# Optimization experiments

Measured on AMD Instinct MI355X. Metric: run time of the kernel, lower is better.

Reference implementation:

```python
import jax, jax.numpy as jnp
import numpy as np
from jax import lax

DEPTH = 3
L = 2 ** DEPTH          # n_leaves
N_NODES = 2 ** DEPTH - 1
B, C, H, W = 256, 3, 32, 32
OC = 64
K = 3
OUT_WIDTH = 10
INPUT_WIDTH = C * H * W
FC_IN = OC * H * W // 4


def setup_inputs() -> dict:
    key = jax.random.key(0)
    ks = jax.random.split(key, 9)
    f1 = 1.0 / np.sqrt(INPUT_WIDTH)
    u = lambda k, shape, f: jax.random.uniform(k, shape, jnp.float32, -f, f)
    fcf = 1.0 / np.sqrt(FC_IN)
    return {
        "x": jax.random.normal(ks[0], (B, C, H, W), jnp.float32),
        "node_weights": u(ks[1], (N_NODES, INPUT_WIDTH), f1),
        "node_biases": u(ks[2], (N_NODES, 1), f1),
        "cw1s": u(ks[3], (L, OC, C, K, K), f1),
        "cb1s": u(ks[4], (L, OC), f1),
        "cw2s": u(ks[5], (L, OC, OC, K, K), f1),
        "cb2s": u(ks[6], (L, OC), f1),
        "fc_w": u(ks[7], (OUT_WIDTH, FC_IN), fcf),
        "fc_b": u(ks[8], (OUT_WIDTH,), fcf),
    }


def _soft_mixture(xf, node_weights, node_biases):
    # xf: [B, C*H*W] -> per-sample mixture over leaves [B, L]
    b = xf.shape[0]
    mixture = jnp.ones((b, L), xf.dtype)
    for d in range(DEPTH):  # fixed small structural loop over tree depth
        p0, p1 = 2 ** d - 1, 2 ** (d + 1) - 1
        n = 2 ** d
        logits = xf @ node_weights[p0:p1].T + node_biases[p0:p1].T  # [B, n]
        be = jax.nn.sigmoid(logits)
        mod = jnp.stack([1.0 - be, be], axis=-1).reshape(b, 2 * n, 1)
        mixture = (mixture.reshape(b, 2 * n, L // (2 * n)) * mod).reshape(b, L)
    return mixture


def reference(x, node_weights, node_biases, cw1s, cb1s, cw2s, cb2s, fc_w, fc_b):
    b = x.shape[0]
    xf = x.reshape(b, -1)
    mixture = _soft_mixture(xf, node_weights, node_biases)  # [B, L]

    pad = K // 2  # 'same' padding for odd kernel, stride 1
    # conv1 for all leaves at once: stack leaf kernels along output channels
    w1 = cw1s.reshape(L * OC, C, K, K)
    y = lax.conv_general_dilated(x, w1, (1, 1), [(pad, pad), (pad, pad)])
    y = y + cb1s.reshape(1, L * OC, 1, 1)            # [B, L*OC, H, W]
    y = lax.reduce_window(y, -jnp.inf, lax.max, (1, 1, 2, 2), (1, 1, 2, 2), "VALID")
    y = jax.nn.relu(y)                                # [B, L*OC, H/2, W/2]
    # conv2 as grouped conv (one group per leaf)
    w2 = cw2s.reshape(L * OC, OC, K, K)
    y = lax.conv_general_dilated(y, w2, (1, 1), [(pad, pad), (pad, pad)],
                                 feature_group_count=L)
    y = jax.nn.relu(y + cb2s.reshape(1, L * OC, 1, 1))
    y = y.reshape(b, L, OC, H // 2, W // 2)
    out = jnp.einsum("bl,blchw->bchw", mixture, y)    # mixture-weighted sum over leaves
    flat = out.reshape(b, -1)
    return flat @ fc_w.T + fc_b                       # [B, OUT_WIDTH]
```

## Files before the change

### kernel.cpp

```cpp
#include <hip/hip_runtime.h>
#include <cstdint>
#include <cstddef>

#define B_ 256
#define IW_ 3072
#define L_ 8
#define NN_ 7
#define FCIN_ 16384
#define OUTW_ 10
#define ICST 40
#define YPLANE (324 * ICST)

typedef short short8 __attribute__((ext_vector_type(8)));
typedef float f32x4 __attribute__((ext_vector_type(4)));

__device__ __forceinline__ ushort f2bf(float x) {
    uint u = __float_as_uint(x);
    return (ushort)((u + 0x7fffu + ((u >> 16) & 1u)) >> 16);
}
__device__ __forceinline__ float bf2f(ushort b) { return __uint_as_float(((uint)b) << 16); }

__global__ __launch_bounds__(256) void k_prep(const float* __restrict__ w1, ushort* __restrict__ w1fr,
                                              const float* __restrict__ w2, ushort* __restrict__ w2r,
                                              const float* __restrict__ x, const float* __restrict__ nw,
                                              const float* __restrict__ nb, float* __restrict__ mix) {
    int blk = blockIdx.x;
    if (blk < 64) {
        int i = blk * 256 + threadIdx.x;
        int j    = i & 7;
        int lane = (i >> 3) & 63;
        int mt   = (i >> 9) & 3;
        int l    = i >> 11;
        int fr = lane & 15, fq = lane >> 4;
        int oc = mt * 16 + fr;
        int k = fq * 8 + j;
        float w = (k < 27) ? w1[(size_t)(l * 64 + oc) * 27 + k] : 0.f;
        w1fr[i] = f2bf(w);
        return;
    }
    if (blk < 1216) {
        int i = (blk - 64) * 256 + threadIdx.x;
        int j     = i & 7;
        int lane  = (i >> 3) & 63;
        int mt    = (i >> 9) & 3;
        int tap   = (i >> 11) % 9;
        int icc   = (i / 18432) & 1;
        int l     = i / 36864;
        int fr = lane & 15, fq = lane >> 4;
        int oc = mt * 16 + fr;
        int ic = icc * 32 + fq * 8 + j;
        float w = w2[(((size_t)l * 64 + oc) * 64 + ic) * 9 + tap];
        w2r[i] = f2bf(w);
        return;
    }
    __shared__ float red[4 * NN_];
    __shared__ float bes[NN_];
    int b = blk - 1216, tid = threadIdx.x;
    const float* xb = x + (size_t)b * IW_;
    float p[NN_];
#pragma unroll
    for (int n = 0; n < NN_; ++n) p[n] = 0.f;
    for (int i = tid; i < IW_; i += 256) {
        float xv = xb[i];
#pragma unroll
        for (int n = 0; n < NN_; ++n) p[n] = fmaf(xv, nw[n * IW_ + i], p[n]);
    }
#pragma unroll
    for (int n = 0; n < NN_; ++n) {
        float v = p[n];
        for (int off = 32; off > 0; off >>= 1) v += __shfl_xor(v, off);
        if ((tid & 63) == 0) red[(tid >> 6) * NN_ + n] = v;
    }
    __syncthreads();
    if (tid < NN_) {
        float s = red[tid] + red[NN_ + tid] + red[2 * NN_ + tid] + red[3 * NN_ + tid] + nb[tid];
        bes[tid] = 1.f / (1.f + expf(-s));
    }
    __syncthreads();
    if (tid < L_) {
        int leaf = tid;
        float b0 = bes[0];
        float t0 = ((leaf >> 2) & 1) ? b0 : 1.f - b0;
        float b1v = bes[1 + ((leaf >> 2) & 1)];
        float t1 = ((leaf >> 1) & 1) ? b1v : 1.f - b1v;
        float b2v = bes[3 + ((leaf >> 1) & 3)];
        float t2 = (leaf & 1) ? b2v : 1.f - b2v;
        mix[b * L_ + leaf] = t0 * t1 * t2;
    }
}

__global__ __launch_bounds__(1024, 1) void k_fused(const float* __restrict__ x,
                                                   const ushort* __restrict__ w1fr,
                                                   const float* __restrict__ cb1,
                                                   const ushort* __restrict__ w2r,
                                                   const float* __restrict__ cb2, const float* __restrict__ mixw,
                                                   float* __restrict__ out1, int boff) {
    __shared__ __align__(16) ushort smem[2 * YPLANE];
    float* xpad = (float*)smem;

    int tid = threadIdx.x;
    int bl = blockIdx.x;
    int b = boff + bl;
    int lane = tid & 63, wid = tid >> 6;
    int fr = lane & 15, fq = lane >> 4;
    int mt = wid >> 2, ng = wid & 3;

    for (int i = tid; i < 3 * 34 * 34; i += 1024) xpad[i] = 0.f;
    __syncthreads();
    for (int i = tid; i < 3072; i += 1024) {
        int ch = i >> 10, rr = (i >> 5) & 31, cc = i & 31;
        xpad[(ch * 34 + rr + 1) * 34 + cc + 1] = x[(size_t)b * IW_ + i];
    }
    __syncthreads();

    short8 Bh[4];
#pragma unroll
    for (int i = 0; i < 4; ++i) {
        int subrow = i >> 1;
        int parity = i & 1;
        int prow = wid * 2 + subrow;
        int pcol = 2 * fr + parity;
#pragma unroll
        for (int j = 0; j < 8; ++j) {
            int k = fq * 8 + j;
            float xv = 0.f;
            if (k < 27) {
                int ic = k / 9;
                int tap = k - ic * 9;
                int dr = tap / 3, dc = tap - dr * 3;
                xv = xpad[(ic * 34 + prow + dr) * 34 + (pcol + dc)];
            }
            Bh[i][j] = (short)f2bf(xv);
        }
    }
    __syncthreads();
    {
        uint4 z; z.x = z.y = z.z = z.w = 0u;
        for (int i = tid; i < (2 * YPLANE) / 8; i += 1024) ((uint4*)smem)[i] = z;
    }
    __syncthreads();

    f32x4 acc[4], oacc[4];
#pragma unroll
    for (int rl = 0; rl < 4; ++rl) { acc[rl] = (f32x4)0.f; oacc[rl] = (f32x4)0.f; }

    auto CONV1 = [&](int s) {
        int l = s >> 1, icc = s & 1;
        ushort* yt = smem + (size_t)(s & 1) * YPLANE;
#pragma unroll
        for (int mt2 = 0; mt2 < 2; ++mt2) {
            int mtg = icc * 2 + mt2;
            short8 ah = *(const short8*)(w1fr + ((size_t)(l * 4 + mtg) * 64 + lane) * 8);
            f32x4 a1[4];
#pragma unroll
            for (int i = 0; i < 4; ++i) {
                f32x4 t = (f32x4)0.f;
                t = __builtin_amdgcn_mfma_f32_16x16x32_bf16(ah, Bh[i], t, 0, 0, 0);
                a1[i] = t;
            }
            float4 bias4 = *(const float4*)(cb1 + l * 64 + mtg * 16 + fq * 4);
            float bb[4] = {bias4.x, bias4.y, bias4.z, bias4.w};
            ushort hb[4];
#pragma unroll
            for (int j2 = 0; j2 < 4; ++j2) {
                float m0 = fmaxf(fmaxf(a1[0][j2], a1[1][j2]), fmaxf(a1[2][j2], a1[3][j2]));
                float v = fmaxf(m0 + bb[j2], 0.f);
                hb[j2] = f2bf(v);
            }
            int off = ((wid + 1) * 18 + (fr + 1)) * ICST + mt2 * 16 + fq * 4;
            uint2 H;
            H.x = (uint)hb[0] | ((uint)hb[1] << 16);
            H.y = (uint)hb[2] | ((uint)hb[3] << 16);
            *(uint2*)&yt[off] = H;
        }
    };

    auto CONV2 = [&](int s) {
        int l = s >> 1, icc = s & 1;
        const ushort* yt = smem + (size_t)(s & 1) * YPLANE;
        const ushort* wbase = w2r + (size_t)(l * 2 + icc) * 18432;
#pragma unroll
        for (int dc = 0; dc < 3; ++dc) {
            short8 Ah[3];
#pragma unroll
            for (int dr = 0; dr < 3; ++dr) {
                int tap = dr * 3 + dc;
                Ah[dr] = *(const short8*)(wbase + ((size_t)(tap * 4 + mt) * 64 + lane) * 8);
            }
#pragma unroll
            for (int rr = 0; rr < 6; ++rr) {
                int off = ((4 * ng + rr) * 18 + (fr + dc)) * ICST + fq * 8;
                short8 bh = *(const short8*)(yt + off);
#pragma unroll
                for (int dr = 0; dr < 3; ++dr) {
                    int rl = rr - dr;
                    if (rl >= 0 && rl < 4) {
                        acc[rl] = __builtin_amdgcn_mfma_f32_16x16x32_bf16(Ah[dr], bh, acc[rl], 0, 0, 0);
                    }
                }
            }
        }
        if (icc) {
            float mx = mixw[(size_t)b * 8 + l];
#pragma unroll
            for (int j = 0; j < 4; ++j) {
                float bias = cb2[l * 64 + mt * 16 + fq * 4 + j];
#pragma unroll
                for (int rl = 0; rl < 4; ++rl) {
                    float v = fmaxf(acc[rl][j] + bias, 0.f);
                    oacc[rl][j] = fmaf(mx, v, oacc[rl][j]);
                    acc[rl][j] = 0.f;
                }
            }
        }
    };

    CONV1(0);
    __syncthreads();
    for (int s = 0; s < 16; ++s) {
        if (s < 15) CONV1(s + 1);
        CONV2(s);
        __syncthreads();
    }

#pragma unroll
    for (int rl = 0; rl < 4; ++rl)
#pragma unroll
        for (int j = 0; j < 4; ++j) {
            int oc = mt * 16 + fq * 4 + j;
            int pos = (4 * ng + rl) * 16 + fr;
            out1[((size_t)bl * 64 + oc) * 256 + pos] = oacc[rl][j];
        }
}

__global__ __launch_bounds__(256) void k_fc(const float* __restrict__ out1, const float* __restrict__ fcw,
                                            const float* __restrict__ fcb, float* __restrict__ out, int boff) {
    __shared__ float red[4][OUTW_];
    int tid = threadIdx.x;
    int bl = blockIdx.x;
    const float4* flat = (const float4*)(out1 + (size_t)bl * FCIN_);
    float pj[OUTW_];
#pragma unroll
    for (int j = 0; j < OUTW_; ++j) pj[j] = 0.f;
    for (int i = tid; i < FCIN_ / 4; i += 256) {
        float4 v = flat[i];
#pragma unroll
        for (int j = 0; j < OUTW_; ++j) {
            float4 w = ((const float4*)(fcw + (size_t)j * FCIN_))[i];
            pj[j] += v.x * w.x + v.y * w.y + v.z * w.z + v.w * w.w;
        }
    }
#pragma unroll
    for (int j = 0; j < OUTW_; ++j) {
        float v = pj[j];
        for (int off = 32; off > 0; off >>= 1) v += __shfl_xor(v, off);
        if ((tid & 63) == 0) red[tid >> 6][j] = v;
    }
    __syncthreads();
    if (tid < OUTW_) {
        float s = red[0][tid] + red[1][tid] + red[2][tid] + red[3][tid] + fcb[tid];
        out[(size_t)(boff + bl) * OUTW_ + tid] = s;
    }
}

extern "C" void kernel_launch(void* const* d_in, const int* in_sizes, int n_in,
                              void* d_out, int out_size, void* d_ws, size_t ws_size,
                              hipStream_t stream) {
    const float* x   = (const float*)d_in[0];
    const float* nw  = (const float*)d_in[1];
    const float* nb  = (const float*)d_in[2];
    const float* w1  = (const float*)d_in[3];
    const float* cb1 = (const float*)d_in[4];
    const float* w2  = (const float*)d_in[5];
    const float* cb2 = (const float*)d_in[6];
    const float* fcw = (const float*)d_in[7];
    const float* fcb = (const float*)d_in[8];
    float* out = (float*)d_out;

    float*  ws   = (float*)d_ws;
    float*  mix  = ws;
    ushort* w1fr = (ushort*)(mix + 2048);
    ushort* w2r  = w1fr + 16384;
    float*  out1 = (float*)(w2r + 294912);

    long avail = (long)ws_size - 630784L;
    int Bc = (int)(avail / 65536L);
    if (Bc > B_) Bc = B_;
    if (Bc < 1) Bc = 1;

    k_prep<<<1472, 256, 0, stream>>>(w1, w1fr, w2, w2r, x, nw, nb, mix);

    for (int boff = 0; boff < B_; boff += Bc) {
        int bc = (B_ - boff < Bc) ? (B_ - boff) : Bc;
        k_fused<<<bc, 1024, 0, stream>>>(x, w1fr, cb1, w2r, cb2, mix, out1, boff);
        k_fc<<<bc, 256, 0, stream>>>(out1, fcw, fcb, out, boff);
    }
}
```

Before: 80.30 us.

## Fuse FC into conv kernel and process full leaf per pipeline stage

Computes all 64 conv1 channels per leaf into a wider LDS tile, so the software pipeline runs 8 leaf stages instead of 16 half-channel stages and needs half as many barriers. The FC layer is moved into the fused kernel: the mixture-weighted output is staged in LDS and dotted against fc weights there, which removes the global out1 round trip, the separate k_fc launch and the batch-chunk loop. In exchange it uses more LDS per block, and each block now does its own FC weight streaming.

```diff
diff --git a/kernel.cpp b/kernel.cpp
--- a/kernel.cpp
+++ b/kernel.cpp
@@ -8,7 +8,7 @@
 #define NN_ 7
 #define FCIN_ 16384
 #define OUTW_ 10
-#define ICST 40
+#define ICST 72
 #define YPLANE (324 * ICST)
 
 typedef short short8 __attribute__((ext_vector_type(8)));
@@ -94,13 +94,13 @@
                                                    const float* __restrict__ cb1,
                                                    const ushort* __restrict__ w2r,
                                                    const float* __restrict__ cb2, const float* __restrict__ mixw,
-                                                   float* __restrict__ out1, int boff) {
+                                                   const float* __restrict__ fcw, const float* __restrict__ fcb,
+                                                   float* __restrict__ out) {
     __shared__ __align__(16) ushort smem[2 * YPLANE];
     float* xpad = (float*)smem;
 
     int tid = threadIdx.x;
-    int bl = blockIdx.x;
-    int b = boff + bl;
+    int b = blockIdx.x;
     int lane = tid & 63, wid = tid >> 6;
     int fr = lane & 15, fq = lane >> 4;
     int mt = wid >> 2, ng = wid & 3;
@@ -144,12 +144,10 @@
 #pragma unroll
     for (int rl = 0; rl < 4; ++rl) { acc[rl] = (f32x4)0.f; oacc[rl] = (f32x4)0.f; }
 
-    auto CONV1 = [&](int s) {
-        int l = s >> 1, icc = s & 1;
-        ushort* yt = smem + (size_t)(s & 1) * YPLANE;
-#pragma unroll
-        for (int mt2 = 0; mt2 < 2; ++mt2) {
-            int mtg = icc * 2 + mt2;
+    auto CONV1 = [&](int l) {
+        ushort* yt = smem + (size_t)(l & 1) * YPLANE;
+#pragma unroll
+        for (int mtg = 0; mtg < 4; ++mtg) {
             short8 ah = *(const short8*)(w1fr + ((size_t)(l * 4 + mtg) * 64 + lane) * 8);
             f32x4 a1[4];
 #pragma unroll
@@ -167,7 +165,7 @@
                 float v = fmaxf(m0 + bb[j2], 0.f);
                 hb[j2] = f2bf(v);
             }
-            int off = ((wid + 1) * 18 + (fr + 1)) * ICST + mt2 * 16 + fq * 4;
+            int off = ((wid + 1) * 18 + (fr + 1)) * ICST + mtg * 16 + fq * 4;
             uint2 H;
             H.x = (uint)hb[0] | ((uint)hb[1] << 16);
             H.y = (uint)hb[2] | ((uint)hb[3] << 16);
@@ -175,91 +173,87 @@
         }
     };
 
-    auto CONV2 = [&](int s) {
-        int l = s >> 1, icc = s & 1;
-        const ushort* yt = smem + (size_t)(s & 1) * YPLANE;
-        const ushort* wbase = w2r + (size_t)(l * 2 + icc) * 18432;
+    auto CONV2 = [&](int l) {
+        const ushort* yt = smem + (size_t)(l & 1) * YPLANE;
 #pragma unroll
         for (int dc = 0; dc < 3; ++dc) {
-            short8 Ah[3];
-#pragma unroll
-            for (int dr = 0; dr < 3; ++dr) {
-                int tap = dr * 3 + dc;
-                Ah[dr] = *(const short8*)(wbase + ((size_t)(tap * 4 + mt) * 64 + lane) * 8);
-            }
-#pragma unroll
-            for (int rr = 0; rr < 6; ++rr) {
-                int off = ((4 * ng + rr) * 18 + (fr + dc)) * ICST + fq * 8;
-                short8 bh = *(const short8*)(yt + off);
+#pragma unroll
+            for (int icc = 0; icc < 2; ++icc) {
+                const ushort* wbase = w2r + (size_t)(l * 2 + icc) * 18432;
+                short8 Ah[3];
 #pragma unroll
                 for (int dr = 0; dr < 3; ++dr) {
-                    int rl = rr - dr;
-                    if (rl >= 0 && rl < 4) {
-                        acc[rl] = __builtin_amdgcn_mfma_f32_16x16x32_bf16(Ah[dr], bh, acc[rl], 0, 0, 0);
+                    int tap = dr * 3 + dc;
+                    Ah[dr] = *(const short8*)(wbase + ((size_t)(tap * 4 + mt) * 64 + lane) * 8);
+                }
+#pragma unroll
+                for (int rr = 0; rr < 6; ++rr) {
+                    int off = ((4 * ng + rr) * 18 + (fr + dc)) * ICST + icc * 32 + fq * 8;
+                    short8 bh = *(const short8*)(yt + off);
+#pragma unroll
+                    for (int dr = 0; dr < 3; ++dr) {
+                        int rl = rr - dr;
+                        if (rl >= 0 && rl < 4) {
+                            acc[rl] = __builtin_amdgcn_mfma_f32_16x16x32_bf16(Ah[dr], bh, acc[rl], 0, 0, 0);
+                        }
                     }
                 }
             }
         }
-        if (icc) {
-            float mx = mixw[(size_t)b * 8 + l];
-#pragma unroll
-            for (int j = 0; j < 4; ++j) {
-                float bias = cb2[l * 64 + mt * 16 + fq * 4 + j];
-#pragma unroll
-                for (int rl = 0; rl < 4; ++rl) {
-                    float v = fmaxf(acc[rl][j] + bias, 0.f);
-                    oacc[rl][j] = fmaf(mx, v, oacc[rl][j]);
-                    acc[rl][j] = 0.f;
-                }
+        float mx = mixw[(size_t)b * 8 + l];
+#pragma unroll
+        for (int j = 0; j < 4; ++j) {
+            float bias = cb2[l * 64 + mt * 16 + fq * 4 + j];
+#pragma unroll
+            for (int rl = 0; rl < 4; ++rl) {
+                float v = fmaxf(acc[rl][j] + bias, 0.f);
+                oacc[rl][j] = fmaf(mx, v, oacc[rl][j]);
+                acc[rl][j] = 0.f;
             }
         }
     };
 
     CONV1(0);
     __syncthreads();
-    for (int s = 0; s < 16; ++s) {
-        if (s < 15) CONV1(s + 1);
-        CONV2(s);
+    for (int l = 0; l < 8; ++l) {
+        if (l < 7) CONV1(l + 1);
+        CONV2(l);
         __syncthreads();
     }
 
+    float* ldsOut = (float*)smem;
+    float* sred   = (float*)smem + FCIN_;
 #pragma unroll
     for (int rl = 0; rl < 4; ++rl)
 #pragma unroll
         for (int j = 0; j < 4; ++j) {
             int oc = mt * 16 + fq * 4 + j;
             int pos = (4 * ng + rl) * 16 + fr;
-            out1[((size_t)bl * 64 + oc) * 256 + pos] = oacc[rl][j];
-        }
-}
-
-__global__ __launch_bounds__(256) void k_fc(const float* __restrict__ out1, const float* __restrict__ fcw,
-                                            const float* __restrict__ fcb, float* __restrict__ out, int boff) {
-    __shared__ float red[4][OUTW_];
-    int tid = threadIdx.x;
-    int bl = blockIdx.x;
-    const float4* flat = (const float4*)(out1 + (size_t)bl * FCIN_);
+            ldsOut[oc * 256 + pos] = oacc[rl][j];
+        }
+    __syncthreads();
     float pj[OUTW_];
 #pragma unroll
     for (int j = 0; j < OUTW_; ++j) pj[j] = 0.f;
-    for (int i = tid; i < FCIN_ / 4; i += 256) {
-        float4 v = flat[i];
-#pragma unroll
-        for (int j = 0; j < OUTW_; ++j) {
-            float4 w = ((const float4*)(fcw + (size_t)j * FCIN_))[i];
-            pj[j] += v.x * w.x + v.y * w.y + v.z * w.z + v.w * w.w;
-        }
-    }
-#pragma unroll
-    for (int j = 0; j < OUTW_; ++j) {
-        float v = pj[j];
+#pragma unroll
+    for (int k = 0; k < 16; ++k) {
+        float yv = ldsOut[k * 1024 + tid];
+#pragma unroll
+        for (int jj = 0; jj < OUTW_; ++jj)
+            pj[jj] = fmaf(yv, fcw[(size_t)jj * FCIN_ + k * 1024 + tid], pj[jj]);
+    }
+#pragma unroll
+    for (int jj = 0; jj < OUTW_; ++jj) {
+        float v = pj[jj];
         for (int off = 32; off > 0; off >>= 1) v += __shfl_xor(v, off);
-        if ((tid & 63) == 0) red[tid >> 6][j] = v;
+        if (lane == 0) sred[wid * OUTW_ + jj] = v;
     }
     __syncthreads();
     if (tid < OUTW_) {
-        float s = red[0][tid] + red[1][tid] + red[2][tid] + red[3][tid] + fcb[tid];
-        out[(size_t)(boff + bl) * OUTW_ + tid] = s;
+        float s = fcb[tid];
+#pragma unroll
+        for (int w = 0; w < 16; ++w) s += sred[w * OUTW_ + tid];
+        out[(size_t)b * OUTW_ + tid] = s;
     }
 }
 
@@ -281,18 +275,7 @@
     float*  mix  = ws;
     ushort* w1fr = (ushort*)(mix + 2048);
     ushort* w2r  = w1fr + 16384;
-    float*  out1 = (float*)(w2r + 294912);
-
-    long avail = (long)ws_size - 630784L;
-    int Bc = (int)(avail / 65536L);
-    if (Bc > B_) Bc = B_;
-    if (Bc < 1) Bc = 1;
 
     k_prep<<<1472, 256, 0, stream>>>(w1, w1fr, w2, w2r, x, nw, nb, mix);
-
-    for (int boff = 0; boff < B_; boff += Bc) {
-        int bc = (B_ - boff < Bc) ? (B_ - boff) : Bc;
-        k_fused<<<bc, 1024, 0, stream>>>(x, w1fr, cb1, w2r, cb2, mix, out1, boff);
-        k_fc<<<bc, 256, 0, stream>>>(out1, fcw, fcb, out, boff);
-    }
-}
+    k_fused<<<B_, 1024, 0, stream>>>(x, w1fr, cb1, w2r, cb2, mix, fcw, fcb, out);
+}
```

New measurement: 104.6 us. +30.2%, slower.
